# Kernel tuning notes

Measured on AMD Instinct MI355X. Metric: run time of the kernel, lower is better.

Reference implementation:

```python
import jax, jax.numpy as jnp
import numpy as np

# Constants derived from init_kwargs: dt, simulation_params = [gamma, omega, n, eta, kappa, b]
DT = 0.001
GAMMA, OMEGA, N_TH, ETA, KAPPA = 0.3, 6.283185, 14.0, 0.8, 0.9
A = jnp.array([[-GAMMA / 2, OMEGA], [-OMEGA, -GAMMA / 2]], dtype=jnp.float32)
C = np.float32(np.sqrt(4 * ETA * KAPPA)) * jnp.array([[1.0, 0.0], [0.0, 0.0]], dtype=jnp.float32)
D = np.float32(GAMMA * (N_TH + 0.5) + KAPPA) * jnp.eye(2, dtype=jnp.float32)
PROJ_F = jnp.array([[0.0, 0.0], [1.0, 0.0]], dtype=jnp.float32)  # squeezed proj_F

B, T = 4096, 2048


def setup_inputs() -> dict:
    key = jax.random.key(0)
    k1, k2, k3 = jax.random.split(key, 3)
    dy = jax.random.normal(k1, (B, T, 2), dtype=jnp.float32) * np.float32(np.sqrt(DT))
    state = jax.random.uniform(k2, (B, 6), dtype=jnp.float32)  # [q, p, Vx, Vp, Cxp, t]
    f = jax.random.normal(k3, (B, 2), dtype=jnp.float32)
    kernel_params = jnp.array([[0.0, 1.0], [-1.0, 0.0]], dtype=jnp.float32)  # trainable 2x2
    return {"dy": dy, "state": state, "f": f, "kernel_params": kernel_params}


def _step(state, f, dy_t, K):
    # state: [B,6], f: [B,2], dy_t: [B,2], K: [2,2]
    x = state[:, :2]
    vx, vp, cxp = state[:, 2], state[:, 3], state[:, 4]
    t = state[:, 5]
    cov = jnp.stack([jnp.stack([vx, cxp], -1), jnp.stack([cxp, vp], -1)], -2)  # [B,2,2]
    xicov = jnp.einsum('bij,kj->bik', cov, C)  # cov @ C.T
    M = A[None] - jnp.einsum('bij,jk->bik', xicov, C)  # A - xicov @ C
    dx = jnp.einsum('bij,bj->bi', M, x) * DT + jnp.einsum('bij,bj->bi', xicov, dy_t)
    fnew = f + jnp.einsum('ij,bj->bi', K, f) * DT
    dx = dx + jnp.einsum('ij,bj->bi', PROJ_F, fnew) * DT
    ncov = cov + DT * (
        jnp.einsum('bij,kj->bik', cov, A)
        + jnp.einsum('ij,bjk->bik', A, cov)
        + D[None]
        - jnp.einsum('bij,bkj->bik', xicov, xicov)
    )
    nstate = jnp.concatenate(
        [x + dx, ncov[:, 0, 0:1], ncov[:, 1, 1:2], ncov[:, 1, 0:1], (t + DT)[:, None]], axis=1
    )
    dy_hat = jnp.einsum('ij,bj->bi', C, x) * DT  # uses OLD x, as in torch code
    return nstate, fnew, dy_hat


def reference(dy, state, f, kernel_params):
    dy_tb = jnp.swapaxes(dy, 0, 1)  # [T,B,2]

    def scan_fn(carry, dyt):
        s, fc = carry
        ns, fn, yh = _step(s, fc, dyt, kernel_params)
        return (ns, fn), yh

    (nstate, fnew), dy_hat = jax.lax.scan(scan_fn, (state, f), dy_tb)
    return nstate, jnp.swapaxes(dy_hat, 0, 1), fnew
```

## Files before the change

kernel.cpp:

```cpp
#include <hip/hip_runtime.h>
#include <cmath>


#define NBATCH 4096
#define NT     2048
#define ROWF4  1024

struct M16 { float m[16]; };

namespace gk {

constexpr float DT   = 0.001f;
constexpr float A00  = -0.15f;
constexpr float A01  = 6.283185f;
constexpr float A10  = -6.283185f;
constexpr float A11  = -0.15f;
constexpr float C0   = 1.6970562748477141f;
constexpr float DD   = 5.25f;

constexpr float P00c = 1.0f + DT*A00;
constexpr float P01c = DT*A01;
constexpr float P10c = DT*A10;
constexpr float P11c = 1.0f + DT*A11;
constexpr float DTC  = DT*C0;
constexpr float QQ   = DT*C0*C0;
constexpr float cVA  = 1.0f + 2.0f*DT*A00;
constexpr float cVB  = 2.0f*DT*A01;
constexpr float cVBn = 2.0f*DT*A10;
constexpr float cVD  = DT*DD;
constexpr float cCA  = 1.0f + DT*(A00+A11);
constexpr float cCB  = DT*A10;
constexpr float cCC  = DT*A01;
constexpr float YC   = C0*DT;

__device__ __forceinline__ void cov_step(float& vx, float& vp, float& cxp)
{
    float a1 = fmaf(-QQ, vx,  cVA);
    float b1 = fmaf(cVB, cxp, cVD);
    float a2 = fmaf(-QQ, cxp, cVBn);
    float b2 = fmaf(a2,  cxp, cVD);
    float a3 = fmaf(-QQ, vx,  cCA);
    float m  = cCC * vp;
    float c3 = fmaf(cCB, vx,  m);
    float nvx = fmaf(a1,  vx,  b1);
    float nvp = fmaf(cVA, vp,  b2);
    float ncx = fmaf(a3,  cxp, c3);
    vx = nvx; vp = nvp; cxp = ncx;
}

__device__ __forceinline__ void covf_step(
    float& vx, float& vp, float& cxp, float& f0, float& f1,
    float k00, float k01, float k10, float k11,
    float& xi0o, float& xi1o, float& nf0o)
{
    float xi0 = C0*vx, xi1 = C0*cxp;
    float nf0 = fmaf(DT, fmaf(k00, f0, k01*f1), f0);
    float nf1 = fmaf(DT, fmaf(k10, f0, k11*f1), f1);
    xi0o = xi0; xi1o = xi1; nf0o = nf0;
    cov_step(vx, vp, cxp);
    f0 = nf0; f1 = nf1;
}

__device__ __forceinline__ void mat4_mul(const float* A, const float* B, float* C)
{
    #pragma unroll
    for (int i = 0; i < 4; ++i)
        #pragma unroll
        for (int j = 0; j < 4; ++j) {
            float acc = A[i*4+0] * B[0*4+j];
            acc = fmaf(A[i*4+1], B[1*4+j], acc);
            acc = fmaf(A[i*4+2], B[2*4+j], acc);
            acc = fmaf(A[i*4+3], B[3*4+j], acc);
            C[i*4+j] = acc;
        }
}

__device__ __forceinline__ void lft_apply(const float* m, float& vx, float& vp, float& cxp)
{
    float n00 = fmaf(m[0], vx,  fmaf(m[1], cxp, m[2]));
    float n01 = fmaf(m[0], cxp, fmaf(m[1], vp,  m[3]));
    float n10 = fmaf(m[4], vx,  fmaf(m[5], cxp, m[6]));
    float n11 = fmaf(m[4], cxp, fmaf(m[5], vp,  m[7]));
    float d00 = fmaf(m[8],  vx,  fmaf(m[9],  cxp, m[10]));
    float d01 = fmaf(m[8],  cxp, fmaf(m[9],  vp,  m[11]));
    float d10 = fmaf(m[12], vx,  fmaf(m[13], cxp, m[14]));
    float d11 = fmaf(m[12], cxp, fmaf(m[13], vp,  m[15]));
    float rdet = 1.0f / fmaf(d00, d11, -d01*d10);
    float p00 = fmaf(n00, d11, -n01*d10) * rdet;
    float p01 = fmaf(n01, d00, -n00*d01) * rdet;
    float p10 = fmaf(n10, d11, -n11*d10) * rdet;
    float p11 = fmaf(n11, d00, -n10*d01) * rdet;
    vx = p00; vp = p11; cxp = 0.5f*(p01 + p10);
}

__device__ __forceinline__ int xcd_swz(int bx, int n)
{
    return (bx & 7) * (n >> 3) + (bx >> 3);
}

}

__global__ void __launch_bounds__(128, 1)
kinit(const float* __restrict__ kp, M16 mlb, float* __restrict__ ws)
{
    using namespace gk;
    const int e = threadIdx.x;

    float acc[16] = {1,0,0,0, 0,1,0,0, 0,0,1,0, 0,0,0,1};
    float bas[16];
    #pragma unroll
    for (int i = 0; i < 16; ++i) bas[i] = mlb.m[i];
    #pragma unroll
    for (int it = 0; it < 7; ++it) {
        float t[16];
        if ((e >> it) & 1) {
            mat4_mul(acc, bas, t);
            #pragma unroll
            for (int i = 0; i < 16; ++i) acc[i] = t[i];
        }
        if (it < 6) {
            mat4_mul(bas, bas, t);
            #pragma unroll
            for (int i = 0; i < 16; ++i) bas[i] = t[i];
        }
    }
    #pragma unroll
    for (int i = 0; i < 16; ++i) ws[e*16 + i] = acc[i];

    float m00 = fmaf(DT,kp[0],1.f), m01 = DT*kp[1];
    float m10 = DT*kp[2],           m11 = fmaf(DT,kp[3],1.f);
    #pragma unroll
    for (int i = 0; i < 4; ++i) {
        float a = fmaf(m00,m00, m01*m10);
        float q = fmaf(m00,m01, m01*m11);
        float c = fmaf(m10,m00, m11*m10);
        float d = fmaf(m10,m01, m11*m11);
        m00=a; m01=q; m10=c; m11=d;
    }
    float a00=1.f, a01=0.f, a10=0.f, a11=1.f;
    #pragma unroll
    for (int it = 0; it < 7; ++it) {
        if ((e >> it) & 1) {
            float x0 = fmaf(a00,m00, a01*m10);
            float x1 = fmaf(a00,m01, a01*m11);
            float x2 = fmaf(a10,m00, a11*m10);
            float x3 = fmaf(a10,m01, a11*m11);
            a00=x0; a01=x1; a10=x2; a11=x3;
        }
        if (it < 6) {
            float x0 = fmaf(m00,m00, m01*m10);
            float x1 = fmaf(m00,m01, m01*m11);
            float x2 = fmaf(m10,m00, m11*m10);
            float x3 = fmaf(m10,m01, m11*m11);
            m00=x0; m01=x1; m10=x2; m11=x3;
        }
    }
    ws[2048 + e*4 + 0] = a00;  ws[2048 + e*4 + 1] = a01;
    ws[2048 + e*4 + 2] = a10;  ws[2048 + e*4 + 3] = a11;
}

__global__ void __launch_bounds__(256, 4)
kfused(const float* __restrict__ dy, const float* __restrict__ state,
       const float* __restrict__ fin, const float* __restrict__ kp,
       const float* __restrict__ ws, float* __restrict__ out)
{
    using namespace gk;
    __shared__ float tsh[2][8];
    const int lane = threadIdx.x & 63;
    const int wv   = threadIdx.x >> 6;
    const int bi   = wv >> 1;
    const int w    = wv & 1;
    const int g    = xcd_swz(blockIdx.x, gridDim.x);
    const int b    = g*2 + bi;
    const int e    = (w << 6) | lane;

    const float k00 = kp[0], k01 = kp[1], k10 = kp[2], k11 = kp[3];
    const float x0i = state[b*6+0], x1i = state[b*6+1];
    const float vx0 = state[b*6+2], vp0 = state[b*6+3], cx0 = state[b*6+4];
    const float t0v = state[b*6+5];
    const float f0i = fin[b*2+0],   f1i = fin[b*2+1];

    float vx = vx0, vp = vp0, cxp = cx0;
    {
        const float4* tml = reinterpret_cast<const float4*>(ws) + e*4;
        float4 q0 = tml[0], q1 = tml[1], q2 = tml[2], q3 = tml[3];
        float m[16] = { q0.x,q0.y,q0.z,q0.w, q1.x,q1.y,q1.z,q1.w,
                        q2.x,q2.y,q2.z,q2.w, q3.x,q3.y,q3.z,q3.w };
        lft_apply(m, vx, vp, cxp);
    }
    float4 fm = reinterpret_cast<const float4*>(ws + 2048)[e];
    float f0 = fmaf(fm.x, f0i, fm.y*f1i);
    float f1 = fmaf(fm.z, f0i, fm.w*f1i);
    const float vxs = vx, vps = vp, cxs = cxp, f0s = f0, f1s = f1;

    const float4* base = reinterpret_cast<const float4*>(dy)
                       + (size_t)b*ROWF4 + w*512 + lane*8;
    float4 v[8];
    #pragma unroll
    for (int j = 0; j < 8; ++j) v[j] = base[j];

    float X00 = 1.f, X01 = 0.f, X10 = 0.f, X11 = 1.f, Q0 = 0.f, Q1 = 0.f;
    #pragma unroll
    for (int j = 0; j < 8; ++j) {
        #pragma unroll
        for (int h = 0; h < 2; ++h) {
            float dy0 = h ? v[j].z : v[j].x;
            float xi0, xi1, nf0;
            covf_step(vx, vp, cxp, f0, f1, k00, k01, k10, k11, xi0, xi1, nf0);
            float p00 = fmaf(-DTC, xi0, P00c);
            float p10 = fmaf(-DTC, xi1, P10c);
            float r0  = xi0*dy0;
            float r1  = fmaf(DT, nf0, xi1*dy0);
            float nX00 = fmaf(p00, X00, P01c*X10);
            float nX01 = fmaf(p00, X01, P01c*X11);
            float nX10 = fmaf(p10, X00, P11c*X10);
            float nX11 = fmaf(p10, X01, P11c*X11);
            float nQ0  = fmaf(p00, Q0, fmaf(P01c, Q1, r0));
            float nQ1  = fmaf(p10, Q0, fmaf(P11c, Q1, r1));
            X00 = nX00; X01 = nX01; X10 = nX10; X11 = nX11; Q0 = nQ0; Q1 = nQ1;
        }
    }

    float A00 = X00, A01 = X01, A10 = X10, A11 = X11, B0 = Q0, B1 = Q1;
    #pragma unroll
    for (int d = 1; d < 64; d <<= 1) {
        float r00 = __shfl_up(A00, d);
        float r01 = __shfl_up(A01, d);
        float r10 = __shfl_up(A10, d);
        float r11 = __shfl_up(A11, d);
        float rB0 = __shfl_up(B0,  d);
        float rB1 = __shfl_up(B1,  d);
        if (lane >= d) {
            float n00 = fmaf(A00, r00, A01*r10);
            float n01 = fmaf(A00, r01, A01*r11);
            float n10 = fmaf(A10, r00, A11*r10);
            float n11 = fmaf(A10, r01, A11*r11);
            float nB0 = fmaf(A00, rB0, fmaf(A01, rB1, B0));
            float nB1 = fmaf(A10, rB0, fmaf(A11, rB1, B1));
            A00=n00; A01=n01; A10=n10; A11=n11; B0=nB0; B1=nB1;
        }
    }

    if (w == 0 && lane == 63) {
        tsh[bi][0]=A00; tsh[bi][1]=A01; tsh[bi][2]=A10;
        tsh[bi][3]=A11; tsh[bi][4]=B0;  tsh[bi][5]=B1;
    }
    __syncthreads();
    float xb0 = x0i, xb1 = x1i;
    if (w == 1) {
        float T00=tsh[bi][0], T01=tsh[bi][1], T10=tsh[bi][2];
        float T11=tsh[bi][3], TB0=tsh[bi][4], TB1=tsh[bi][5];
        xb0 = fmaf(T00, x0i, fmaf(T01, x1i, TB0));
        xb1 = fmaf(T10, x0i, fmaf(T11, x1i, TB1));
    }

    float e00 = __shfl_up(A00, 1);
    float e01 = __shfl_up(A01, 1);
    float e10 = __shfl_up(A10, 1);
    float e11 = __shfl_up(A11, 1);
    float eB0 = __shfl_up(B0,  1);
    float eB1 = __shfl_up(B1,  1);
    float x0 = (lane == 0) ? xb0 : fmaf(e00, xb0, fmaf(e01, xb1, eB0));
    float x1 = (lane == 0) ? xb1 : fmaf(e10, xb0, fmaf(e11, xb1, eB1));

    vx = vxs; vp = vps; cxp = cxs; f0 = f0s; f1 = f1s;
    #pragma unroll
    for (int j = 0; j < 8; ++j) {
        float yh0, yh1;
        #pragma unroll
        for (int h = 0; h < 2; ++h) {
            float dy0 = h ? v[j].z : v[j].x;
            float yh  = YC * x0;
            if (h) yh1 = yh; else yh0 = yh;
            float xi0, xi1, nf0;
            covf_step(vx, vp, cxp, f0, f1, k00, k01, k10, k11, xi0, xi1, nf0);
            float p00 = fmaf(-DTC, xi0, P00c);
            float p10 = fmaf(-DTC, xi1, P10c);
            float r0  = xi0*dy0;
            float r1  = fmaf(DT, nf0, xi1*dy0);
            float nx0 = fmaf(p00, x0, fmaf(P01c, x1, r0));
            float nx1 = fmaf(p10, x0, fmaf(P11c, x1, r1));
            x0 = nx0; x1 = nx1;
        }
        v[j] = make_float4(yh0, 0.f, yh1, 0.f);
    }

    float4* dst = reinterpret_cast<float4*>(out + 6*NBATCH)
                + (size_t)b*ROWF4 + w*512 + lane*8;
    #pragma unroll
    for (int j = 0; j < 8; ++j) dst[j] = v[j];

    if (w == 1 && lane == 63) {
        out[b*6+0] = x0; out[b*6+1] = x1;
        out[b*6+2] = vx; out[b*6+3] = vp; out[b*6+4] = cxp;
        out[b*6+5] = t0v + 2.048f;
        float* fo = out + 6*NBATCH + (size_t)NBATCH*NT*2;
        fo[b*2+0] = f0; fo[b*2+1] = f1;
    }
}

static M16 build_m_pow(int log2n)
{
    const double dt = 0.001;
    const double a00 = -0.15, a01 = 6.283185, a10 = -6.283185, a11 = -0.15;
    const double qq = dt * 4.0 * 0.8 * 0.9;
    const double qd = dt * 5.25;
    const double h00 = 1.0 + dt*a00, h01 = dt*a01;
    const double h10 = dt*a10,       h11 = 1.0 + dt*a11;
    const double det = h00*h11 - h01*h10;
    const double t00 = h11/det, t01 = -h10/det, t10 = -h01/det, t11 = h00/det;
    const double g00 = t00*qq, g10 = t10*qq;
    double M[4][4] = {
        { h00 + qd*g00, h01, qd*t00, qd*t01 },
        { h10 + qd*g10, h11, qd*t10, qd*t11 },
        { g00,          0.0, t00,    t01    },
        { g10,          0.0, t10,    t11    },
    };
    for (int it = 0; it < log2n; ++it) {
        double R[4][4];
        for (int i = 0; i < 4; ++i)
            for (int j = 0; j < 4; ++j) {
                double acc = 0.0;
                for (int k = 0; k < 4; ++k) acc += M[i][k]*M[k][j];
                R[i][j] = acc;
            }
        for (int i = 0; i < 4; ++i)
            for (int j = 0; j < 4; ++j) M[i][j] = R[i][j];
    }
    M16 r;
    for (int i = 0; i < 4; ++i)
        for (int j = 0; j < 4; ++j) r.m[i*4+j] = (float)M[i][j];
    return r;
}

extern "C" void kernel_launch(void* const* d_in, const int* in_sizes, int n_in,
                              void* d_out, int out_size, void* d_ws, size_t ws_size,
                              hipStream_t stream)
{
    const float* dy    = (const float*)d_in[0];
    const float* state = (const float*)d_in[1];
    const float* fin   = (const float*)d_in[2];
    const float* kp    = (const float*)d_in[3];
    float* out = (float*)d_out;
    float* ws  = (float*)d_ws;

    M16 mlb = build_m_pow(4);

    kinit<<<dim3(1), dim3(128), 0, stream>>>(kp, mlb, ws);
    kfused<<<dim3(NBATCH/2), dim3(256), 0, stream>>>(dy, state, fin, kp, ws, out);
}
```

Measured before the change: 50.05 us.

## Map each batch row to one wavefront with 32 steps per lane

Each batch row is now handled by a single 64-lane wavefront, with every lane processing 32 timesteps instead of 16. This removes the cross-wave shared-memory handoff and the __syncthreads. Each wave loops over two batch rows, the grid shrinks to 512 blocks, and the precomputed covariance and f propagators now cover 32-step strides. The trade-offs are a longer serial chain per lane, more registers (16 float4 buffered loads), lower occupancy, and dy loads for the second row that are not overlapped with compute.

```diff
diff --git a/kernel.cpp b/kernel.cpp
--- a/kernel.cpp
+++ b/kernel.cpp
@@ -100,7 +100,7 @@
 
 }
 
-__global__ void __launch_bounds__(128, 1)
+__global__ void __launch_bounds__(64, 1)
 kinit(const float* __restrict__ kp, M16 mlb, float* __restrict__ ws)
 {
     using namespace gk;
@@ -111,14 +111,14 @@
     #pragma unroll
     for (int i = 0; i < 16; ++i) bas[i] = mlb.m[i];
     #pragma unroll
-    for (int it = 0; it < 7; ++it) {
+    for (int it = 0; it < 6; ++it) {
         float t[16];
         if ((e >> it) & 1) {
             mat4_mul(acc, bas, t);
             #pragma unroll
             for (int i = 0; i < 16; ++i) acc[i] = t[i];
         }
-        if (it < 6) {
+        if (it < 5) {
             mat4_mul(bas, bas, t);
             #pragma unroll
             for (int i = 0; i < 16; ++i) bas[i] = t[i];
@@ -130,7 +130,7 @@
     float m00 = fmaf(DT,kp[0],1.f), m01 = DT*kp[1];
     float m10 = DT*kp[2],           m11 = fmaf(DT,kp[3],1.f);
     #pragma unroll
-    for (int i = 0; i < 4; ++i) {
+    for (int i = 0; i < 5; ++i) {
         float a = fmaf(m00,m00, m01*m10);
         float q = fmaf(m00,m01, m01*m11);
         float c = fmaf(m10,m00, m11*m10);
@@ -139,7 +139,7 @@
     }
     float a00=1.f, a01=0.f, a10=0.f, a11=1.f;
     #pragma unroll
-    for (int it = 0; it < 7; ++it) {
+    for (int it = 0; it < 6; ++it) {
         if ((e >> it) & 1) {
             float x0 = fmaf(a00,m00, a01*m10);
             float x1 = fmaf(a00,m01, a01*m11);
@@ -147,7 +147,7 @@
             float x3 = fmaf(a10,m01, a11*m11);
             a00=x0; a01=x1; a10=x2; a11=x3;
         }
-        if (it < 6) {
+        if (it < 5) {
             float x0 = fmaf(m00,m00, m01*m10);
             float x1 = fmaf(m00,m01, m01*m11);
             float x2 = fmaf(m10,m00, m11*m10);
@@ -155,147 +155,141 @@
             m00=x0; m01=x1; m10=x2; m11=x3;
         }
     }
-    ws[2048 + e*4 + 0] = a00;  ws[2048 + e*4 + 1] = a01;
-    ws[2048 + e*4 + 2] = a10;  ws[2048 + e*4 + 3] = a11;
-}
-
-__global__ void __launch_bounds__(256, 4)
+    ws[1024 + e*4 + 0] = a00;  ws[1024 + e*4 + 1] = a01;
+    ws[1024 + e*4 + 2] = a10;  ws[1024 + e*4 + 3] = a11;
+}
+
+__global__ void __launch_bounds__(256, 2)
 kfused(const float* __restrict__ dy, const float* __restrict__ state,
        const float* __restrict__ fin, const float* __restrict__ kp,
        const float* __restrict__ ws, float* __restrict__ out)
 {
     using namespace gk;
-    __shared__ float tsh[2][8];
     const int lane = threadIdx.x & 63;
     const int wv   = threadIdx.x >> 6;
-    const int bi   = wv >> 1;
-    const int w    = wv & 1;
     const int g    = xcd_swz(blockIdx.x, gridDim.x);
-    const int b    = g*2 + bi;
-    const int e    = (w << 6) | lane;
+    const int W    = g*4 + wv;
 
     const float k00 = kp[0], k01 = kp[1], k10 = kp[2], k11 = kp[3];
-    const float x0i = state[b*6+0], x1i = state[b*6+1];
-    const float vx0 = state[b*6+2], vp0 = state[b*6+3], cx0 = state[b*6+4];
-    const float t0v = state[b*6+5];
-    const float f0i = fin[b*2+0],   f1i = fin[b*2+1];
-
-    float vx = vx0, vp = vp0, cxp = cx0;
+
+    float m[16];
     {
-        const float4* tml = reinterpret_cast<const float4*>(ws) + e*4;
+        const float4* tml = reinterpret_cast<const float4*>(ws) + lane*4;
         float4 q0 = tml[0], q1 = tml[1], q2 = tml[2], q3 = tml[3];
-        float m[16] = { q0.x,q0.y,q0.z,q0.w, q1.x,q1.y,q1.z,q1.w,
-                        q2.x,q2.y,q2.z,q2.w, q3.x,q3.y,q3.z,q3.w };
+        m[0]=q0.x; m[1]=q0.y; m[2]=q0.z; m[3]=q0.w;
+        m[4]=q1.x; m[5]=q1.y; m[6]=q1.z; m[7]=q1.w;
+        m[8]=q2.x; m[9]=q2.y; m[10]=q2.z; m[11]=q2.w;
+        m[12]=q3.x; m[13]=q3.y; m[14]=q3.z; m[15]=q3.w;
+    }
+    const float4 fm = reinterpret_cast<const float4*>(ws + 1024)[lane];
+
+    float4 v[16];
+
+    #pragma unroll 1
+    for (int iter = 0; iter < 2; ++iter) {
+        const int b = 2*W + iter;
+
+        const float x0i = state[b*6+0], x1i = state[b*6+1];
+        const float vx0 = state[b*6+2], vp0 = state[b*6+3], cx0 = state[b*6+4];
+        const float t0v = state[b*6+5];
+        const float f0i = fin[b*2+0],   f1i = fin[b*2+1];
+
+        const float4* base = reinterpret_cast<const float4*>(dy)
+                           + (size_t)b*ROWF4 + lane*16;
+        #pragma unroll
+        for (int j = 0; j < 16; ++j) v[j] = base[j];
+
+        float vx = vx0, vp = vp0, cxp = cx0;
         lft_apply(m, vx, vp, cxp);
-    }
-    float4 fm = reinterpret_cast<const float4*>(ws + 2048)[e];
-    float f0 = fmaf(fm.x, f0i, fm.y*f1i);
-    float f1 = fmaf(fm.z, f0i, fm.w*f1i);
-    const float vxs = vx, vps = vp, cxs = cxp, f0s = f0, f1s = f1;
-
-    const float4* base = reinterpret_cast<const float4*>(dy)
-                       + (size_t)b*ROWF4 + w*512 + lane*8;
-    float4 v[8];
-    #pragma unroll
-    for (int j = 0; j < 8; ++j) v[j] = base[j];
-
-    float X00 = 1.f, X01 = 0.f, X10 = 0.f, X11 = 1.f, Q0 = 0.f, Q1 = 0.f;
-    #pragma unroll
-    for (int j = 0; j < 8; ++j) {
-        #pragma unroll
-        for (int h = 0; h < 2; ++h) {
-            float dy0 = h ? v[j].z : v[j].x;
-            float xi0, xi1, nf0;
-            covf_step(vx, vp, cxp, f0, f1, k00, k01, k10, k11, xi0, xi1, nf0);
-            float p00 = fmaf(-DTC, xi0, P00c);
-            float p10 = fmaf(-DTC, xi1, P10c);
-            float r0  = xi0*dy0;
-            float r1  = fmaf(DT, nf0, xi1*dy0);
-            float nX00 = fmaf(p00, X00, P01c*X10);
-            float nX01 = fmaf(p00, X01, P01c*X11);
-            float nX10 = fmaf(p10, X00, P11c*X10);
-            float nX11 = fmaf(p10, X01, P11c*X11);
-            float nQ0  = fmaf(p00, Q0, fmaf(P01c, Q1, r0));
-            float nQ1  = fmaf(p10, Q0, fmaf(P11c, Q1, r1));
-            X00 = nX00; X01 = nX01; X10 = nX10; X11 = nX11; Q0 = nQ0; Q1 = nQ1;
-        }
-    }
-
-    float A00 = X00, A01 = X01, A10 = X10, A11 = X11, B0 = Q0, B1 = Q1;
-    #pragma unroll
-    for (int d = 1; d < 64; d <<= 1) {
-        float r00 = __shfl_up(A00, d);
-        float r01 = __shfl_up(A01, d);
-        float r10 = __shfl_up(A10, d);
-        float r11 = __shfl_up(A11, d);
-        float rB0 = __shfl_up(B0,  d);
-        float rB1 = __shfl_up(B1,  d);
-        if (lane >= d) {
-            float n00 = fmaf(A00, r00, A01*r10);
-            float n01 = fmaf(A00, r01, A01*r11);
-            float n10 = fmaf(A10, r00, A11*r10);
-            float n11 = fmaf(A10, r01, A11*r11);
-            float nB0 = fmaf(A00, rB0, fmaf(A01, rB1, B0));
-            float nB1 = fmaf(A10, rB0, fmaf(A11, rB1, B1));
-            A00=n00; A01=n01; A10=n10; A11=n11; B0=nB0; B1=nB1;
-        }
-    }
-
-    if (w == 0 && lane == 63) {
-        tsh[bi][0]=A00; tsh[bi][1]=A01; tsh[bi][2]=A10;
-        tsh[bi][3]=A11; tsh[bi][4]=B0;  tsh[bi][5]=B1;
-    }
-    __syncthreads();
-    float xb0 = x0i, xb1 = x1i;
-    if (w == 1) {
-        float T00=tsh[bi][0], T01=tsh[bi][1], T10=tsh[bi][2];
-        float T11=tsh[bi][3], TB0=tsh[bi][4], TB1=tsh[bi][5];
-        xb0 = fmaf(T00, x0i, fmaf(T01, x1i, TB0));
-        xb1 = fmaf(T10, x0i, fmaf(T11, x1i, TB1));
-    }
-
-    float e00 = __shfl_up(A00, 1);
-    float e01 = __shfl_up(A01, 1);
-    float e10 = __shfl_up(A10, 1);
-    float e11 = __shfl_up(A11, 1);
-    float eB0 = __shfl_up(B0,  1);
-    float eB1 = __shfl_up(B1,  1);
-    float x0 = (lane == 0) ? xb0 : fmaf(e00, xb0, fmaf(e01, xb1, eB0));
-    float x1 = (lane == 0) ? xb1 : fmaf(e10, xb0, fmaf(e11, xb1, eB1));
-
-    vx = vxs; vp = vps; cxp = cxs; f0 = f0s; f1 = f1s;
-    #pragma unroll
-    for (int j = 0; j < 8; ++j) {
-        float yh0, yh1;
-        #pragma unroll
-        for (int h = 0; h < 2; ++h) {
-            float dy0 = h ? v[j].z : v[j].x;
-            float yh  = YC * x0;
-            if (h) yh1 = yh; else yh0 = yh;
-            float xi0, xi1, nf0;
-            covf_step(vx, vp, cxp, f0, f1, k00, k01, k10, k11, xi0, xi1, nf0);
-            float p00 = fmaf(-DTC, xi0, P00c);
-            float p10 = fmaf(-DTC, xi1, P10c);
-            float r0  = xi0*dy0;
-            float r1  = fmaf(DT, nf0, xi1*dy0);
-            float nx0 = fmaf(p00, x0, fmaf(P01c, x1, r0));
-            float nx1 = fmaf(p10, x0, fmaf(P11c, x1, r1));
-            x0 = nx0; x1 = nx1;
-        }
-        v[j] = make_float4(yh0, 0.f, yh1, 0.f);
-    }
-
-    float4* dst = reinterpret_cast<float4*>(out + 6*NBATCH)
-                + (size_t)b*ROWF4 + w*512 + lane*8;
-    #pragma unroll
-    for (int j = 0; j < 8; ++j) dst[j] = v[j];
-
-    if (w == 1 && lane == 63) {
-        out[b*6+0] = x0; out[b*6+1] = x1;
-        out[b*6+2] = vx; out[b*6+3] = vp; out[b*6+4] = cxp;
-        out[b*6+5] = t0v + 2.048f;
-        float* fo = out + 6*NBATCH + (size_t)NBATCH*NT*2;
-        fo[b*2+0] = f0; fo[b*2+1] = f1;
+        float f0 = fmaf(fm.x, f0i, fm.y*f1i);
+        float f1 = fmaf(fm.z, f0i, fm.w*f1i);
+        const float vxs = vx, vps = vp, cxs = cxp, f0s = f0, f1s = f1;
+
+        float X00 = 1.f, X01 = 0.f, X10 = 0.f, X11 = 1.f, Q0 = 0.f, Q1 = 0.f;
+        #pragma unroll
+        for (int j = 0; j < 16; ++j) {
+            #pragma unroll
+            for (int h = 0; h < 2; ++h) {
+                float dy0 = h ? v[j].z : v[j].x;
+                float xi0, xi1, nf0;
+                covf_step(vx, vp, cxp, f0, f1, k00, k01, k10, k11, xi0, xi1, nf0);
+                float p00 = fmaf(-DTC, xi0, P00c);
+                float p10 = fmaf(-DTC, xi1, P10c);
+                float r0  = xi0*dy0;
+                float r1  = fmaf(DT, nf0, xi1*dy0);
+                float nX00 = fmaf(p00, X00, P01c*X10);
+                float nX01 = fmaf(p00, X01, P01c*X11);
+                float nX10 = fmaf(p10, X00, P11c*X10);
+                float nX11 = fmaf(p10, X01, P11c*X11);
+                float nQ0  = fmaf(p00, Q0, fmaf(P01c, Q1, r0));
+                float nQ1  = fmaf(p10, Q0, fmaf(P11c, Q1, r1));
+                X00 = nX00; X01 = nX01; X10 = nX10; X11 = nX11; Q0 = nQ0; Q1 = nQ1;
+            }
+        }
+
+        float A00 = X00, A01 = X01, A10 = X10, A11 = X11, B0 = Q0, B1 = Q1;
+        #pragma unroll
+        for (int d = 1; d < 64; d <<= 1) {
+            float r00 = __shfl_up(A00, d);
+            float r01 = __shfl_up(A01, d);
+            float r10 = __shfl_up(A10, d);
+            float r11 = __shfl_up(A11, d);
+            float rB0 = __shfl_up(B0,  d);
+            float rB1 = __shfl_up(B1,  d);
+            if (lane >= d) {
+                float n00 = fmaf(A00, r00, A01*r10);
+                float n01 = fmaf(A00, r01, A01*r11);
+                float n10 = fmaf(A10, r00, A11*r10);
+                float n11 = fmaf(A10, r01, A11*r11);
+                float nB0 = fmaf(A00, rB0, fmaf(A01, rB1, B0));
+                float nB1 = fmaf(A10, rB0, fmaf(A11, rB1, B1));
+                A00=n00; A01=n01; A10=n10; A11=n11; B0=nB0; B1=nB1;
+            }
+        }
+        float e00 = __shfl_up(A00, 1);
+        float e01 = __shfl_up(A01, 1);
+        float e10 = __shfl_up(A10, 1);
+        float e11 = __shfl_up(A11, 1);
+        float eB0 = __shfl_up(B0,  1);
+        float eB1 = __shfl_up(B1,  1);
+        float x0 = (lane == 0) ? x0i : fmaf(e00, x0i, fmaf(e01, x1i, eB0));
+        float x1 = (lane == 0) ? x1i : fmaf(e10, x0i, fmaf(e11, x1i, eB1));
+
+        float vx2 = vxs, vp2 = vps, cx2 = cxs;
+        f0 = f0s; f1 = f1s;
+        #pragma unroll
+        for (int j = 0; j < 16; ++j) {
+            float yh0, yh1;
+            #pragma unroll
+            for (int h = 0; h < 2; ++h) {
+                float dy0 = h ? v[j].z : v[j].x;
+                float yh  = YC * x0;
+                if (h) yh1 = yh; else yh0 = yh;
+                float xi0, xi1, nf0;
+                covf_step(vx2, vp2, cx2, f0, f1, k00, k01, k10, k11, xi0, xi1, nf0);
+                float p00 = fmaf(-DTC, xi0, P00c);
+                float p10 = fmaf(-DTC, xi1, P10c);
+                float r0  = xi0*dy0;
+                float r1  = fmaf(DT, nf0, xi1*dy0);
+                float nx0 = fmaf(p00, x0, fmaf(P01c, x1, r0));
+                float nx1 = fmaf(p10, x0, fmaf(P11c, x1, r1));
+                x0 = nx0; x1 = nx1;
+            }
+            v[j] = make_float4(yh0, 0.f, yh1, 0.f);
+        }
+
+        float4* dst = reinterpret_cast<float4*>(out + 6*NBATCH)
+                    + (size_t)b*ROWF4 + lane*16;
+        #pragma unroll
+        for (int j = 0; j < 16; ++j) dst[j] = v[j];
+
+        if (lane == 63) {
+            out[b*6+0] = x0; out[b*6+1] = x1;
+            out[b*6+2] = vx2; out[b*6+3] = vp2; out[b*6+4] = cx2;
+            out[b*6+5] = t0v + 2.048f;
+            float* fo = out + 6*NBATCH + (size_t)NBATCH*NT*2;
+            fo[b*2+0] = f0; fo[b*2+1] = f1;
+        }
     }
 }
 
@@ -344,8 +338,8 @@
     float* out = (float*)d_out;
     float* ws  = (float*)d_ws;
 
-    M16 mlb = build_m_pow(4);
-
-    kinit<<<dim3(1), dim3(128), 0, stream>>>(kp, mlb, ws);
-    kfused<<<dim3(NBATCH/2), dim3(256), 0, stream>>>(dy, state, fin, kp, ws, out);
-}
+    M16 mlb = build_m_pow(5);
+
+    kinit<<<dim3(1), dim3(64), 0, stream>>>(kp, mlb, ws);
+    kfused<<<dim3(512), dim3(256), 0, stream>>>(dy, state, fin, kp, ws, out);
+}
```

Measured after the change: 53.09 us. 6.1% more time.
